# Kernel optimization log

Hardware: AMD Instinct MI355X
Metric: run time of the kernel (lower is better)

## Reference

```python
import jax, jax.numpy as jnp
import numpy as np

B, L, H, HD, FD = 1, 1024, 32, 64, 64
HID = H * HD
EPS = 1e-12


def setup_inputs() -> dict:
    key = jax.random.key(0)
    ks = jax.random.split(key, 7)
    s = 1.0 / np.sqrt(HID)
    return {
        "hidden_states": jax.random.normal(ks[0], (B, L, HID), dtype=jnp.float32),
        "Wq": jax.random.normal(ks[1], (HID, HID), dtype=jnp.float32) * s,
        "Wk": jax.random.normal(ks[2], (HID, HID), dtype=jnp.float32) * s,
        "Wv": jax.random.normal(ks[3], (HID, HID), dtype=jnp.float32) * s,
        "Wo": jax.random.normal(ks[4], (HID, HID), dtype=jnp.float32) * s,
        "Wfq": jax.random.normal(ks[5], (H, HD, FD), dtype=jnp.float32) * (1.0 / np.sqrt(HD)),
        "Wfk": jax.random.normal(ks[6], (H, HD, FD), dtype=jnp.float32) * (1.0 / np.sqrt(HD)),
    }


def _heads(x):
    # [b, l, hid] -> [b, h, l, hd]
    b, l, _ = x.shape
    return x.reshape(b, l, H, HD).transpose(0, 2, 1, 3)


def _feature_map(x, Wf):
    # per-head learned kernel + softmax over feature dim (hedgehog-style)
    z = jnp.einsum('bhld,hdf->bhlf', x, Wf)
    return jax.nn.softmax(z, axis=-1)


def _linear_attention(q, k, v, eps=EPS):
    # causal_dot_product: cumsum of outer-product KV state (fp32)
    qf, kf, vf = q.astype(jnp.float32), k.astype(jnp.float32), v.astype(jnp.float32)
    kv = jnp.cumsum(jnp.einsum('bhlf,bhld->bhlfd', kf, vf), axis=2)  # [b,h,l,f,d]
    y = jnp.einsum('bhlf,bhlfd->bhld', qf, kv)
    # fp32_attention=False branch: normalizer computed on cumsum(k)
    k_cum = jnp.cumsum(kf, axis=2).astype(q.dtype)
    denom = jnp.einsum('bhld,bhld->bhl', q, k_cum) + eps
    return y.astype(q.dtype) / denom[..., None]


def reference(hidden_states, Wq, Wk, Wv, Wo, Wfq, Wfk):
    b, l, _ = hidden_states.shape
    q = _heads(hidden_states @ Wq.T)
    k = _heads(hidden_states @ Wk.T)
    v = _heads(hidden_states @ Wv.T)
    fq = _feature_map(q, Wfq)
    fk = _feature_map(k, Wfk)
    y = _linear_attention(fq, fk, v)  # [b,h,l,hd]
    y = y.transpose(0, 2, 1, 3).reshape(b, l, HID)
    return y @ Wo.T
```

## Files before the change

### kernel.cpp

```cpp
#include <hip/hip_runtime.h>
#include <math.h>

constexpr int LQ  = 1024;
constexpr int NH  = 32;
constexpr int HDM = 64;
constexpr int FDM = 64;
constexpr int HID = 2048;
constexpr int NCH = 16;
constexpr int CT  = 64;
#define EPSV 1e-12f

typedef __bf16 bf16x8 __attribute__((ext_vector_type(8)));
typedef float  f32x4  __attribute__((ext_vector_type(4)));

__device__ __forceinline__ unsigned short f2b_raw(float x) {
    union { float f; unsigned int u; } v; v.f = x;
    unsigned int r = v.u + 0x7fffu + ((v.u >> 16) & 1u);
    return (unsigned short)(r >> 16);
}
__device__ __forceinline__ float b2f(ushort u) {
    union { unsigned int i; float f; } v; v.i = ((unsigned int)u) << 16; return v.f;
}

#define ASYNC16(ldsp, gp) __builtin_amdgcn_global_load_lds( \
    (const __attribute__((address_space(1))) void*)(gp),    \
    (__attribute__((address_space(3))) void*)(ldsp), 16, 0, 0)

template <int TM, int TN, bool BF16OUT>
__device__ __forceinline__ void gemm_core(const ushort* __restrict__ A,
                                          const ushort* __restrict__ B,
                                          void* __restrict__ Cv,
                                          int M, int N, int K) {
    constexpr int FI = TM / 32, FJ = TN / 32;
    constexpr int AI = TM / 32, BJ = TN / 32;
    constexpr int ASZ = TM * 64, BSZ = TN * 64;
    __shared__ __align__(16) ushort As[2 * ASZ];
    __shared__ __align__(16) ushort Bs[2 * BSZ];

    const int t = threadIdx.x, wave = t >> 6, lane = t & 63;
    const int wr = (wave >> 1) * (TM / 2), wc = (wave & 1) * (TN / 2);
    const int bm = blockIdx.y * TM, bn = blockIdx.x * TN;

    const int grow = lane >> 3;
    const int gsw  = ((lane & 7) ^ (grow & 7)) << 3;
    const int arow0 = wave * (TM / 4), brow0 = wave * (TN / 4);
    const ushort* gA = A + (size_t)(bm + arow0 + grow) * K + gsw;
    const ushort* gB = B + (size_t)(bn + brow0 + grow) * K + gsw;

    const int fr = lane & 15, q = lane >> 4;

    f32x4 acc[FI][FJ] = {};
    const int NIT = K >> 6;

    {
        ushort* ab = As + arow0 * 64;
        ushort* bb = Bs + brow0 * 64;
#pragma unroll
        for (int i = 0; i < AI; ++i) ASYNC16(ab + i * 512, gA + (size_t)i * 8 * K);
#pragma unroll
        for (int j = 0; j < BJ; ++j) ASYNC16(bb + j * 512, gB + (size_t)j * 8 * K);
    }
    __syncthreads();

    for (int it = 0; it < NIT; ++it) {
        const int p = it & 1;
        if (it + 1 < NIT) {
            const int ko = (it + 1) << 6;
            ushort* ab = As + (p ^ 1) * ASZ + arow0 * 64;
            ushort* bb = Bs + (p ^ 1) * BSZ + brow0 * 64;
#pragma unroll
            for (int i = 0; i < AI; ++i) ASYNC16(ab + i * 512, gA + ko + (size_t)i * 8 * K);
#pragma unroll
            for (int j = 0; j < BJ; ++j) ASYNC16(bb + j * 512, gB + ko + (size_t)j * 8 * K);
        }
        const ushort* ap = As + p * ASZ;
        const ushort* bp = Bs + p * BSZ;
        bf16x8 af[2][FI], bg[2][FJ];
#pragma unroll
        for (int ks = 0; ks < 2; ++ks) {
#pragma unroll
            for (int i = 0; i < FI; ++i) {
                const int row = wr + i * 16 + fr;
                af[ks][i] = *(const bf16x8*)&ap[row * 64 + ((((q + ks * 4)) ^ (row & 7)) << 3)];
            }
#pragma unroll
            for (int j = 0; j < FJ; ++j) {
                const int row = wc + j * 16 + fr;
                bg[ks][j] = *(const bf16x8*)&bp[row * 64 + ((((q + ks * 4)) ^ (row & 7)) << 3)];
            }
        }
#pragma unroll
        for (int ks = 0; ks < 2; ++ks)
#pragma unroll
            for (int i = 0; i < FI; ++i)
#pragma unroll
                for (int j = 0; j < FJ; ++j)
                    acc[i][j] = __builtin_amdgcn_mfma_f32_16x16x32_bf16(af[ks][i], bg[ks][j], acc[i][j], 0, 0, 0);
        if (it + 1 < NIT) __syncthreads();
    }

    const int er = q * 4;
    const int ec = lane & 15;
#pragma unroll
    for (int i = 0; i < FI; ++i)
#pragma unroll
        for (int j = 0; j < FJ; ++j) {
            const size_t base = (size_t)(bm + wr + i * 16 + er) * N + bn + wc + j * 16 + ec;
            if constexpr (BF16OUT) {
                ushort* C = (ushort*)Cv;
#pragma unroll
                for (int r = 0; r < 4; ++r) C[base + (size_t)r * N] = f2b_raw(acc[i][j][r]);
            } else {
                float* C = (float*)Cv;
#pragma unroll
                for (int r = 0; r < 4; ++r) C[base + (size_t)r * N] = acc[i][j][r];
            }
        }
}

__global__ __launch_bounds__(256) void gemm_qkv(const ushort* __restrict__ hsb,
                                                const ushort* __restrict__ wqb,
                                                const ushort* __restrict__ wkb,
                                                const ushort* __restrict__ wvb,
                                                ushort* __restrict__ qb,
                                                ushort* __restrict__ kb,
                                                ushort* __restrict__ vb) {
    const ushort* B; ushort* C;
    if (blockIdx.z == 0)      { B = wqb; C = qb; }
    else if (blockIdx.z == 1) { B = wkb; C = kb; }
    else                      { B = wvb; C = vb; }
    gemm_core<64, 128, true>(hsb, B, C, LQ, HID, HID);
}

__global__ __launch_bounds__(256) void gemm_one(const ushort* __restrict__ A,
                                                const ushort* __restrict__ B,
                                                float* __restrict__ C) {
    gemm_core<64, 64, false>(A, B, C, LQ, HID, HID);
}

struct F2BArgs { const float* src[5]; ushort* dst[5]; int n[5]; };
__global__ __launch_bounds__(256) void f2b_multi(F2BArgs p) {
    const int which = blockIdx.y;
    const float* s = p.src[which];
    ushort* d = p.dst[which];
    const int n = p.n[which];
    const int i = (blockIdx.x * 256 + threadIdx.x) * 4;
    if (i >= n) return;
    float4 v = *(const float4*)&s[i];
    ushort4 o = make_ushort4(f2b_raw(v.x), f2b_raw(v.y), f2b_raw(v.z), f2b_raw(v.w));
    *(ushort4*)&d[i] = o;
}

__global__ __launch_bounds__(256) void wf_transpose(const float* __restrict__ Wfq,
                                                    const float* __restrict__ Wfk,
                                                    ushort* __restrict__ WfqT,
                                                    ushort* __restrict__ WfkT) {
    const int h = blockIdx.x, isK = blockIdx.y;
    const float* src = (isK ? Wfk : Wfq) + (size_t)h * 4096;
    ushort* dst = (isK ? WfkT : WfqT) + (size_t)h * 4096;
    __shared__ float tile[64][65];
    const int t = threadIdx.x;
    for (int it = 0; it < 16; ++it) {
        int e = it * 256 + t; int d = e >> 6, f = e & 63;
        tile[d][f] = src[e];
    }
    __syncthreads();
    for (int it = 0; it < 16; ++it) {
        int e = it * 256 + t; int f = e >> 6, d = e & 63;
        dst[e] = f2b_raw(tile[d][f]);
    }
}

__global__ __launch_bounds__(256) void featmap_chunk(
    const ushort* __restrict__ qb, const ushort* __restrict__ kb,
    const ushort* __restrict__ vb,
    const ushort* __restrict__ WfqT, const ushort* __restrict__ WfkT,
    ushort* __restrict__ fqB, ushort* __restrict__ fkB,
    ushort* __restrict__ VTb, float* __restrict__ Sraw, float* __restrict__ Ks) {
    __shared__ __align__(16) ushort Xs[64 * 72];
    __shared__ __align__(16) ushort Ws[64 * 72];
    __shared__ float Zs[64][68];
    __shared__ __align__(16) ushort Fs[64 * 72];
    __shared__ __align__(16) ushort Vs[64 * 72];

    const int c = blockIdx.x, h = blockIdx.y, isK = blockIdx.z;
    const int t = threadIdx.x, lane = t & 63, wave = t >> 6;
    const int l0 = c * CT;
    const int fr = lane & 15, fo = (lane >> 4) * 8;
    const int g = lane >> 4, cc = lane & 15;

    const ushort* X  = (isK ? kb : qb);
    const ushort* WT = (isK ? WfkT : WfqT) + (size_t)h * 4096;

    for (int it = 0; it < 2; ++it) {
        int e = (it * 256 + t) * 8;
        int row = e >> 6, col = e & 63;
        *(uint4*)&Xs[row * 72 + col] = *(const uint4*)&X[(size_t)(l0 + row) * HID + h * HDM + col];
        *(uint4*)&Ws[row * 72 + col] = *(const uint4*)&WT[e];
        if (isK) {
            uint4 vv = *(const uint4*)&vb[(size_t)(l0 + row) * HID + h * HDM + col];
            const ushort* pv = (const ushort*)&vv;
#pragma unroll
            for (int i = 0; i < 8; ++i) Vs[(col + i) * 72 + row] = pv[i];
        }
    }
    __syncthreads();

    f32x4 accZ[4] = {};
#pragma unroll
    for (int kp = 0; kp < 2; ++kp) {
        bf16x8 a = *(const bf16x8*)&Xs[(wave * 16 + fr) * 72 + kp * 32 + fo];
#pragma unroll
        for (int j = 0; j < 4; ++j) {
            bf16x8 b = *(const bf16x8*)&Ws[(j * 16 + fr) * 72 + kp * 32 + fo];
            accZ[j] = __builtin_amdgcn_mfma_f32_16x16x32_bf16(a, b, accZ[j], 0, 0, 0);
        }
    }
#pragma unroll
    for (int j = 0; j < 4; ++j)
#pragma unroll
        for (int r = 0; r < 4; ++r)
            Zs[wave * 16 + g * 4 + r][j * 16 + cc] = accZ[j][r];
    __syncthreads();

    const int srow = t >> 2, spart = t & 3;
    float zv[16], m = -1e30f;
#pragma unroll
    for (int i = 0; i < 16; ++i) { zv[i] = Zs[srow][spart * 16 + i]; m = fmaxf(m, zv[i]); }
    m = fmaxf(m, __shfl_xor(m, 1)); m = fmaxf(m, __shfl_xor(m, 2));
    float s = 0.f;
#pragma unroll
    for (int i = 0; i < 16; ++i) { zv[i] = __expf(zv[i] - m); s += zv[i]; }
    s += __shfl_xor(s, 1); s += __shfl_xor(s, 2);
    const float inv = 1.0f / s;
    ushort ov[16];
#pragma unroll
    for (int i = 0; i < 16; ++i) ov[i] = f2b_raw(zv[i] * inv);
    ushort* outp = (isK ? fkB : fqB) + ((size_t)h * LQ + l0 + srow) * FDM + spart * 16;
    *(uint4*)&outp[0] = *(uint4*)&ov[0];
    *(uint4*)&outp[8] = *(uint4*)&ov[8];
    if (isK) {
#pragma unroll
        for (int i = 0; i < 16; ++i) Fs[(spart * 16 + i) * 72 + srow] = ov[i];
    }
    if (!isK) return;
    __syncthreads();

    if (t < 64) {
        float ks = 0.f;
#pragma unroll 8
        for (int l = 0; l < 64; ++l) ks += b2f(Fs[t * 72 + l]);
        Ks[((size_t)h * NCH + c) * FDM + t] = ks;
    }
    const size_t cb = ((size_t)h * NCH + c) * 4096;
    for (int it = 0; it < 2; ++it) {
        int e = (it * 256 + t) * 8;
        int row = e >> 6, col = e & 63;
        *(uint4*)&VTb[cb + e] = *(const uint4*)&Vs[row * 72 + col];
    }
    f32x4 accS[4] = {};
#pragma unroll
    for (int kp = 0; kp < 2; ++kp) {
        bf16x8 a = *(const bf16x8*)&Vs[(wave * 16 + fr) * 72 + kp * 32 + fo];
#pragma unroll
        for (int j = 0; j < 4; ++j) {
            bf16x8 b = *(const bf16x8*)&Fs[(j * 16 + fr) * 72 + kp * 32 + fo];
            accS[j] = __builtin_amdgcn_mfma_f32_16x16x32_bf16(a, b, accS[j], 0, 0, 0);
        }
    }
    float* sp = Sraw + cb;
#pragma unroll
    for (int j = 0; j < 4; ++j)
#pragma unroll
        for (int r = 0; r < 4; ++r)
            sp[(wave * 16 + g * 4 + r) * 64 + j * 16 + cc] = accS[j][r];
}

__global__ __launch_bounds__(256) void prefix2(const float* __restrict__ Sraw,
                                               ushort* __restrict__ SpreB,
                                               const float* __restrict__ Ks,
                                               float* __restrict__ Kpre) {
    const int h = blockIdx.x, eb = blockIdx.y, t = threadIdx.x;
    const int e0 = eb * 512 + t * 2;
    float r0 = 0.f, r1 = 0.f;
    const size_t hb = (size_t)h * NCH * 4096;
    for (int c2 = 0; c2 < NCH; ++c2) {
        const size_t base = hb + (size_t)c2 * 4096 + e0;
        float c0 = Sraw[base], c1 = Sraw[base + 1];
        ushort2 o = make_ushort2(f2b_raw(r0), f2b_raw(r1));
        *(ushort2*)&SpreB[base] = o;
        r0 += c0; r1 += c1;
    }
    if (eb == 0 && t < 64) {
        float rk = 0.f;
        for (int c2 = 0; c2 < NCH; ++c2) {
            const size_t kb2 = ((size_t)h * NCH + c2) * FDM + t;
            float cur = Ks[kb2];
            Kpre[kb2] = rk;
            rk += cur;
        }
    }
}

__global__ __launch_bounds__(256) void intra2(
    const ushort* __restrict__ fqB, const ushort* __restrict__ fkB,
    const ushort* __restrict__ VTb, const ushort* __restrict__ SpreB,
    const float* __restrict__ Kpre, ushort* __restrict__ Yb) {
    __shared__ __align__(16) ushort fqs[64 * 72];
    __shared__ __align__(16) ushort fks[64 * 72];
    __shared__ __align__(16) ushort VTs[64 * 72];
    __shared__ __align__(16) ushort Sps[64 * 72];
    __shared__ __align__(16) ushort Pms[64 * 72];
    __shared__ float den[64], kpr[64];

    const int c = blockIdx.x, h = blockIdx.y;
    const int t = threadIdx.x, lane = t & 63, wave = t >> 6;
    const int l0 = c * CT;
    const int fr = lane & 15, fo = (lane >> 4) * 8;
    const int g = lane >> 4, cc = lane & 15;

    const size_t qkbase = ((size_t)h * LQ + l0) * FDM;
    const size_t cbase  = ((size_t)h * NCH + c) * 4096;
    for (int it = 0; it < 2; ++it) {
        int e = (it * 256 + t) * 8;
        int row = e >> 6, col = e & 63;
        *(uint4*)&fqs[row * 72 + col] = *(const uint4*)&fqB[qkbase + e];
        *(uint4*)&fks[row * 72 + col] = *(const uint4*)&fkB[qkbase + e];
        *(uint4*)&VTs[row * 72 + col] = *(const uint4*)&VTb[cbase + e];
        *(uint4*)&Sps[row * 72 + col] = *(const uint4*)&SpreB[cbase + e];
    }
    if (t < 64) kpr[t] = Kpre[((size_t)h * NCH + c) * FDM + t];
    __syncthreads();

    f32x4 accP[4] = {};
#pragma unroll
    for (int kp = 0; kp < 2; ++kp) {
        bf16x8 a = *(const bf16x8*)&fqs[(wave * 16 + fr) * 72 + kp * 32 + fo];
#pragma unroll
        for (int j = 0; j < 4; ++j) {
            bf16x8 b = *(const bf16x8*)&fks[(j * 16 + fr) * 72 + kp * 32 + fo];
            accP[j] = __builtin_amdgcn_mfma_f32_16x16x32_bf16(a, b, accP[j], 0, 0, 0);
        }
    }
#pragma unroll
    for (int j = 0; j < 4; ++j)
#pragma unroll
        for (int r = 0; r < 4; ++r) {
            int l = wave * 16 + g * 4 + r, lp = j * 16 + cc;
            Pms[l * 72 + lp] = (lp <= l) ? f2b_raw(accP[j][r]) : (ushort)0;
        }
    __syncthreads();

    {
        const int srow = t >> 2, spart = t & 3;
        float s = 0.f;
#pragma unroll
        for (int i = 0; i < 16; ++i) s += b2f(Pms[srow * 72 + spart * 16 + i]);
#pragma unroll
        for (int i = 0; i < 16; ++i) s += b2f(fqs[srow * 72 + spart * 16 + i]) * kpr[spart * 16 + i];
        s += __shfl_xor(s, 1); s += __shfl_xor(s, 2);
        if (spart == 0) den[srow] = s + EPSV;
    }
    __syncthreads();

    f32x4 accY[4] = {};
#pragma unroll
    for (int kp = 0; kp < 2; ++kp) {
        bf16x8 a = *(const bf16x8*)&Pms[(wave * 16 + fr) * 72 + kp * 32 + fo];
#pragma unroll
        for (int j = 0; j < 4; ++j) {
            bf16x8 b = *(const bf16x8*)&VTs[(j * 16 + fr) * 72 + kp * 32 + fo];
            accY[j] = __builtin_amdgcn_mfma_f32_16x16x32_bf16(a, b, accY[j], 0, 0, 0);
        }
    }
#pragma unroll
    for (int kp = 0; kp < 2; ++kp) {
        bf16x8 a = *(const bf16x8*)&fqs[(wave * 16 + fr) * 72 + kp * 32 + fo];
#pragma unroll
        for (int j = 0; j < 4; ++j) {
            bf16x8 b = *(const bf16x8*)&Sps[(j * 16 + fr) * 72 + kp * 32 + fo];
            accY[j] = __builtin_amdgcn_mfma_f32_16x16x32_bf16(a, b, accY[j], 0, 0, 0);
        }
    }
#pragma unroll
    for (int r = 0; r < 4; ++r) {
        int l = wave * 16 + g * 4 + r;
        float inv = 1.0f / den[l];
        ushort* yo = Yb + (size_t)(l0 + l) * HID + h * HDM;
#pragma unroll
        for (int j = 0; j < 4; ++j)
            yo[j * 16 + cc] = f2b_raw(accY[j][r] * inv);
    }
}

extern "C" void kernel_launch(void* const* d_in, const int* in_sizes, int n_in,
                              void* d_out, int out_size, void* d_ws, size_t ws_size,
                              hipStream_t stream) {
    const float* hs  = (const float*)d_in[0];
    const float* Wq  = (const float*)d_in[1];
    const float* Wk  = (const float*)d_in[2];
    const float* Wv  = (const float*)d_in[3];
    const float* Wo  = (const float*)d_in[4];
    const float* Wfq = (const float*)d_in[5];
    const float* Wfk = (const float*)d_in[6];
    float* out = (float*)d_out;

    const size_t SZ = (size_t)LQ * HID;
    const size_t WZ = (size_t)HID * HID;

    char* w = (char*)d_ws;
    auto aus = [&](size_t n) { ushort* p = (ushort*)w; w += n * sizeof(ushort); return p; };
    auto afl = [&](size_t n) { float*  p = (float*)w;  w += n * sizeof(float);  return p; };

    ushort* hsb   = aus(SZ);
    ushort* wqb   = aus(WZ);
    ushort* wkb   = aus(WZ);
    ushort* wvb   = aus(WZ);
    ushort* wob   = aus(WZ);
    ushort* qb2   = aus(SZ);
    ushort* kb2   = aus(SZ);
    ushort* vb2   = aus(SZ);
    ushort* fqB   = aus(SZ);
    ushort* fkB   = aus(SZ);
    ushort* VTb   = aus(SZ);
    ushort* WfqT  = aus((size_t)NH * 4096);
    ushort* WfkT  = aus((size_t)NH * 4096);
    ushort* SpreB = aus(SZ);
    ushort* Yb    = aus(SZ);
    float*  Sraw  = afl(SZ);
    float*  Ks    = afl((size_t)NH * NCH * FDM);
    float*  Kpre  = afl((size_t)NH * NCH * FDM);

    F2BArgs fa;
    fa.src[0] = hs; fa.dst[0] = hsb; fa.n[0] = (int)SZ;
    fa.src[1] = Wq; fa.dst[1] = wqb; fa.n[1] = (int)WZ;
    fa.src[2] = Wk; fa.dst[2] = wkb; fa.n[2] = (int)WZ;
    fa.src[3] = Wv; fa.dst[3] = wvb; fa.n[3] = (int)WZ;
    fa.src[4] = Wo; fa.dst[4] = wob; fa.n[4] = (int)WZ;
    f2b_multi<<<dim3((unsigned)(WZ / 1024), 5), 256, 0, stream>>>(fa);

    wf_transpose<<<dim3(NH, 2), 256, 0, stream>>>(Wfq, Wfk, WfqT, WfkT);

    gemm_qkv<<<dim3(HID / 128, LQ / 64, 3), 256, 0, stream>>>(hsb, wqb, wkb, wvb, qb2, kb2, vb2);

    featmap_chunk<<<dim3(NCH, NH, 2), 256, 0, stream>>>(qb2, kb2, vb2, WfqT, WfkT,
                                                        fqB, fkB, VTb, Sraw, Ks);

    prefix2<<<dim3(NH, 8), 256, 0, stream>>>(Sraw, SpreB, Ks, Kpre);

    intra2<<<dim3(NCH, NH), 256, 0, stream>>>(fqB, fkB, VTb, SpreB, Kpre, Yb);

    gemm_one<<<dim3(HID / 64, LQ / 64), 256, 0, stream>>>(Yb, wob, out);
}
```

Measured before the change: 198.5 us.

## Fuse feature-map softmax into QKV GEMM epilogue and merge conversion kernels

```diff
diff --git a/kernel.cpp b/kernel.cpp
--- a/kernel.cpp
+++ b/kernel.cpp
@@ -81,12 +81,12 @@
 #pragma unroll
             for (int i = 0; i < FI; ++i) {
                 const int row = wr + i * 16 + fr;
-                af[ks][i] = *(const bf16x8*)&ap[row * 64 + ((((q + ks * 4)) ^ (row & 7)) << 3)];
+                af[ks][i] = *(const bf16x8*)&ap[row * 64 + (((q + ks * 4) ^ (row & 7)) << 3)];
             }
 #pragma unroll
             for (int j = 0; j < FJ; ++j) {
                 const int row = wc + j * 16 + fr;
-                bg[ks][j] = *(const bf16x8*)&bp[row * 64 + ((((q + ks * 4)) ^ (row & 7)) << 3)];
+                bg[ks][j] = *(const bf16x8*)&bp[row * 64 + (((q + ks * 4) ^ (row & 7)) << 3)];
             }
         }
 #pragma unroll
@@ -99,8 +99,7 @@
         if (it + 1 < NIT) __syncthreads();
     }
 
-    const int er = q * 4;
-    const int ec = lane & 15;
+    const int er = q * 4, ec = lane & 15;
 #pragma unroll
     for (int i = 0; i < FI; ++i)
 #pragma unroll
@@ -118,48 +117,189 @@
         }
 }
 
-__global__ __launch_bounds__(256) void gemm_qkv(const ushort* __restrict__ hsb,
-                                                const ushort* __restrict__ wqb,
-                                                const ushort* __restrict__ wkb,
-                                                const ushort* __restrict__ wvb,
-                                                ushort* __restrict__ qb,
-                                                ushort* __restrict__ kb,
-                                                ushort* __restrict__ vb) {
-    const ushort* B; ushort* C;
-    if (blockIdx.z == 0)      { B = wqb; C = qb; }
-    else if (blockIdx.z == 1) { B = wkb; C = kb; }
-    else                      { B = wvb; C = vb; }
-    gemm_core<64, 128, true>(hsb, B, C, LQ, HID, HID);
-}
-
 __global__ __launch_bounds__(256) void gemm_one(const ushort* __restrict__ A,
                                                 const ushort* __restrict__ B,
                                                 float* __restrict__ C) {
     gemm_core<64, 64, false>(A, B, C, LQ, HID, HID);
 }
 
-struct F2BArgs { const float* src[5]; ushort* dst[5]; int n[5]; };
-__global__ __launch_bounds__(256) void f2b_multi(F2BArgs p) {
-    const int which = blockIdx.y;
-    const float* s = p.src[which];
-    ushort* d = p.dst[which];
-    const int n = p.n[which];
-    const int i = (blockIdx.x * 256 + threadIdx.x) * 4;
-    if (i >= n) return;
-    float4 v = *(const float4*)&s[i];
-    ushort4 o = make_ushort4(f2b_raw(v.x), f2b_raw(v.y), f2b_raw(v.z), f2b_raw(v.w));
-    *(ushort4*)&d[i] = o;
-}
-
-__global__ __launch_bounds__(256) void wf_transpose(const float* __restrict__ Wfq,
-                                                    const float* __restrict__ Wfk,
-                                                    ushort* __restrict__ WfqT,
-                                                    ushort* __restrict__ WfkT) {
-    const int h = blockIdx.x, isK = blockIdx.y;
-    const float* src = (isK ? Wfk : Wfq) + (size_t)h * 4096;
-    ushort* dst = (isK ? WfkT : WfqT) + (size_t)h * 4096;
+__global__ __launch_bounds__(256) void gemm_qkv_fm(
+    const ushort* __restrict__ hsb,
+    const ushort* __restrict__ wqb, const ushort* __restrict__ wkb,
+    const ushort* __restrict__ wvb,
+    const ushort* __restrict__ WfqT, const ushort* __restrict__ WfkT,
+    ushort* __restrict__ fqB, ushort* __restrict__ fkB,
+    ushort* __restrict__ VTb) {
+    constexpr int TM = 64, TN = 128;
+    constexpr int ASZ = TM * 64, BSZ = TN * 64;
+    __shared__ __align__(16) ushort lds[2 * ASZ + 2 * BSZ];
+    ushort* As = lds;
+    ushort* Bs = lds + 2 * ASZ;
+
+    const int z = blockIdx.z;
+    const ushort* Bmat = (z == 0) ? wqb : (z == 1) ? wkb : wvb;
+
+    const int t = threadIdx.x, wave = t >> 6, lane = t & 63;
+    const int wr = (wave >> 1) * 32, wc = (wave & 1) * 64;
+    const int bx = blockIdx.x, c = blockIdx.y;
+    const int bm = c * TM, bn = bx * TN, l0 = c * CT;
+
+    const int grow = lane >> 3;
+    const int gsw  = ((lane & 7) ^ (grow & 7)) << 3;
+    const int arow0 = wave * 16, brow0 = wave * 32;
+    const ushort* gA = hsb  + (size_t)(bm + arow0 + grow) * HID + gsw;
+    const ushort* gB = Bmat + (size_t)(bn + brow0 + grow) * HID + gsw;
+
+    const int fr = lane & 15, q = lane >> 4, ec = lane & 15;
+
+    f32x4 acc[2][4] = {};
+    const int NIT = HID >> 6;
+
+    {
+        ushort* ab = As + arow0 * 64;
+        ushort* bb = Bs + brow0 * 64;
+#pragma unroll
+        for (int i = 0; i < 2; ++i) ASYNC16(ab + i * 512, gA + (size_t)i * 8 * HID);
+#pragma unroll
+        for (int j = 0; j < 4; ++j) ASYNC16(bb + j * 512, gB + (size_t)j * 8 * HID);
+    }
+    __syncthreads();
+
+    for (int it = 0; it < NIT; ++it) {
+        const int p = it & 1;
+        if (it + 1 < NIT) {
+            const int ko = (it + 1) << 6;
+            ushort* ab = As + (p ^ 1) * ASZ + arow0 * 64;
+            ushort* bb = Bs + (p ^ 1) * BSZ + brow0 * 64;
+#pragma unroll
+            for (int i = 0; i < 2; ++i) ASYNC16(ab + i * 512, gA + ko + (size_t)i * 8 * HID);
+#pragma unroll
+            for (int j = 0; j < 4; ++j) ASYNC16(bb + j * 512, gB + ko + (size_t)j * 8 * HID);
+        }
+        const ushort* ap = As + p * ASZ;
+        const ushort* bp = Bs + p * BSZ;
+        bf16x8 af[2][2], bg[2][4];
+#pragma unroll
+        for (int ks = 0; ks < 2; ++ks) {
+#pragma unroll
+            for (int i = 0; i < 2; ++i) {
+                const int row = wr + i * 16 + fr;
+                af[ks][i] = *(const bf16x8*)&ap[row * 64 + (((q + ks * 4) ^ (row & 7)) << 3)];
+            }
+#pragma unroll
+            for (int j = 0; j < 4; ++j) {
+                const int row = wc + j * 16 + fr;
+                bg[ks][j] = *(const bf16x8*)&bp[row * 64 + (((q + ks * 4) ^ (row & 7)) << 3)];
+            }
+        }
+#pragma unroll
+        for (int ks = 0; ks < 2; ++ks)
+#pragma unroll
+            for (int i = 0; i < 2; ++i)
+#pragma unroll
+                for (int j = 0; j < 4; ++j)
+                    acc[i][j] = __builtin_amdgcn_mfma_f32_16x16x32_bf16(af[ks][i], bg[ks][j], acc[i][j], 0, 0, 0);
+        if (it + 1 < NIT) __syncthreads();
+    }
+
+    if (z == 2) {
+#pragma unroll
+        for (int i = 0; i < 2; ++i)
+#pragma unroll
+            for (int j = 0; j < 4; ++j) {
+                const int col = wc + j * 16 + ec;
+                const int hh = col >> 6, d = col & 63;
+                const int lb = wr + i * 16 + q * 4;
+                const size_t base = (((size_t)(2 * bx + hh) * NCH + c) * 64 + d) * 64 + lb;
+                ushort4 o = make_ushort4(f2b_raw(acc[i][j][0]), f2b_raw(acc[i][j][1]),
+                                         f2b_raw(acc[i][j][2]), f2b_raw(acc[i][j][3]));
+                *(ushort4*)&VTb[base] = o;
+            }
+        return;
+    }
+
+    __syncthreads();
+    ushort* Qt  = lds;
+    ushort* Wfs = lds + 8704;
+#pragma unroll
+    for (int i = 0; i < 2; ++i)
+#pragma unroll
+        for (int j = 0; j < 4; ++j)
+#pragma unroll
+            for (int r = 0; r < 4; ++r)
+                Qt[(wr + i * 16 + q * 4 + r) * 136 + wc + j * 16 + ec] = f2b_raw(acc[i][j][r]);
+    {
+        const ushort* WT = ((z == 0) ? WfqT : WfkT) + (size_t)(2 * bx) * 4096;
+#pragma unroll
+        for (int it = 0; it < 4; ++it) {
+            const int e = it * 2048 + t * 8;
+            const int hh = e >> 12, f = (e >> 6) & 63, dc = e & 63;
+            uint4 wv4 = *(const uint4*)&WT[e];
+            *(uint4*)&Wfs[hh * 4608 + f * 72 + dc] = wv4;
+        }
+    }
+    __syncthreads();
+
+    const int hh = wave & 1, R0 = (wave >> 1) * 32;
+    f32x4 z2[2][4] = {};
+#pragma unroll
+    for (int ks = 0; ks < 2; ++ks) {
+        bf16x8 a[2];
+#pragma unroll
+        for (int i = 0; i < 2; ++i)
+            a[i] = *(const bf16x8*)&Qt[(R0 + i * 16 + fr) * 136 + hh * 64 + ks * 32 + q * 8];
+#pragma unroll
+        for (int j = 0; j < 4; ++j) {
+            bf16x8 b = *(const bf16x8*)&Wfs[hh * 4608 + (j * 16 + fr) * 72 + ks * 32 + q * 8];
+#pragma unroll
+            for (int i = 0; i < 2; ++i)
+                z2[i][j] = __builtin_amdgcn_mfma_f32_16x16x32_bf16(a[i], b, z2[i][j], 0, 0, 0);
+        }
+    }
+
+    ushort* outp = (z == 0) ? fqB : fkB;
+    const int hgl = 2 * bx + hh;
+#pragma unroll
+    for (int i = 0; i < 2; ++i)
+#pragma unroll
+        for (int r = 0; r < 4; ++r) {
+            float m = z2[i][0][r];
+#pragma unroll
+            for (int j = 1; j < 4; ++j) m = fmaxf(m, z2[i][j][r]);
+            m = fmaxf(m, __shfl_xor(m, 1)); m = fmaxf(m, __shfl_xor(m, 2));
+            m = fmaxf(m, __shfl_xor(m, 4)); m = fmaxf(m, __shfl_xor(m, 8));
+            float e4[4], s = 0.f;
+#pragma unroll
+            for (int j = 0; j < 4; ++j) { e4[j] = __expf(z2[i][j][r] - m); s += e4[j]; }
+            s += __shfl_xor(s, 1); s += __shfl_xor(s, 2);
+            s += __shfl_xor(s, 4); s += __shfl_xor(s, 8);
+            const float inv = 1.0f / s;
+            const int l = R0 + i * 16 + q * 4 + r;
+            ushort* op = outp + ((size_t)hgl * LQ + l0 + l) * FDM;
+#pragma unroll
+            for (int j = 0; j < 4; ++j) op[j * 16 + ec] = f2b_raw(e4[j] * inv);
+        }
+}
+
+struct ConvArgs {
+    const float* src[5]; ushort* dst[5]; int n[5];
+    const float* Wfq; const float* Wfk; ushort* WfqT; ushort* WfkT;
+};
+__global__ __launch_bounds__(256) void conv_all(ConvArgs p) {
+    const int y = blockIdx.y, t = threadIdx.x;
+    if (y < 5) {
+        const int i = (blockIdx.x * 256 + t) * 4;
+        if (i >= p.n[y]) return;
+        float4 v = *(const float4*)&p.src[y][i];
+        ushort4 o = make_ushort4(f2b_raw(v.x), f2b_raw(v.y), f2b_raw(v.z), f2b_raw(v.w));
+        *(ushort4*)&p.dst[y][i] = o;
+        return;
+    }
+    if (blockIdx.x >= NH) return;
+    const int h = blockIdx.x;
+    const float* src = ((y == 6) ? p.Wfk : p.Wfq) + (size_t)h * 4096;
+    ushort* dst = ((y == 6) ? p.WfkT : p.WfqT) + (size_t)h * 4096;
     __shared__ float tile[64][65];
-    const int t = threadIdx.x;
     for (int it = 0; it < 16; ++it) {
         int e = it * 256 + t; int d = e >> 6, f = e & 63;
         tile[d][f] = src[e];
@@ -171,109 +311,50 @@
     }
 }
 
-__global__ __launch_bounds__(256) void featmap_chunk(
-    const ushort* __restrict__ qb, const ushort* __restrict__ kb,
-    const ushort* __restrict__ vb,
-    const ushort* __restrict__ WfqT, const ushort* __restrict__ WfkT,
-    ushort* __restrict__ fqB, ushort* __restrict__ fkB,
-    ushort* __restrict__ VTb, float* __restrict__ Sraw, float* __restrict__ Ks) {
-    __shared__ __align__(16) ushort Xs[64 * 72];
-    __shared__ __align__(16) ushort Ws[64 * 72];
-    __shared__ float Zs[64][68];
+__global__ __launch_bounds__(256) void chunk_state(
+    const ushort* __restrict__ fkB, const ushort* __restrict__ VTb,
+    float* __restrict__ Sraw, float* __restrict__ Ks) {
+    __shared__ __align__(16) ushort Vs[64 * 72];
     __shared__ __align__(16) ushort Fs[64 * 72];
-    __shared__ __align__(16) ushort Vs[64 * 72];
-
-    const int c = blockIdx.x, h = blockIdx.y, isK = blockIdx.z;
-    const int t = threadIdx.x, lane = t & 63, wave = t >> 6;
+    const int c = blockIdx.x, h = blockIdx.y;
+    const int t = threadIdx.x, lane = t & 63, w = t >> 6;
     const int l0 = c * CT;
-    const int fr = lane & 15, fo = (lane >> 4) * 8;
-    const int g = lane >> 4, cc = lane & 15;
-
-    const ushort* X  = (isK ? kb : qb);
-    const ushort* WT = (isK ? WfkT : WfqT) + (size_t)h * 4096;
+    const int fr = lane & 15, q = lane >> 4, ec = lane & 15;
+    const size_t cb = ((size_t)h * NCH + c) * 4096;
 
     for (int it = 0; it < 2; ++it) {
-        int e = (it * 256 + t) * 8;
-        int row = e >> 6, col = e & 63;
-        *(uint4*)&Xs[row * 72 + col] = *(const uint4*)&X[(size_t)(l0 + row) * HID + h * HDM + col];
-        *(uint4*)&Ws[row * 72 + col] = *(const uint4*)&WT[e];
-        if (isK) {
-            uint4 vv = *(const uint4*)&vb[(size_t)(l0 + row) * HID + h * HDM + col];
-            const ushort* pv = (const ushort*)&vv;
-#pragma unroll
-            for (int i = 0; i < 8; ++i) Vs[(col + i) * 72 + row] = pv[i];
-        }
-    }
-    __syncthreads();
-
-    f32x4 accZ[4] = {};
-#pragma unroll
-    for (int kp = 0; kp < 2; ++kp) {
-        bf16x8 a = *(const bf16x8*)&Xs[(wave * 16 + fr) * 72 + kp * 32 + fo];
+        const int e = (it * 256 + t) * 8;
+        const int row = e >> 6, col = e & 63;
+        *(uint4*)&Vs[row * 72 + col] = *(const uint4*)&VTb[cb + e];
+        uint4 fv = *(const uint4*)&fkB[((size_t)h * LQ + l0) * FDM + e];
+        const ushort* pf = (const ushort*)&fv;
+#pragma unroll
+        for (int i2 = 0; i2 < 8; ++i2) Fs[(col + i2) * 72 + row] = pf[i2];
+    }
+    __syncthreads();
+
+    f32x4 acc[4] = {};
+#pragma unroll
+    for (int ks = 0; ks < 2; ++ks) {
+        bf16x8 a = *(const bf16x8*)&Vs[(w * 16 + fr) * 72 + ks * 32 + q * 8];
 #pragma unroll
         for (int j = 0; j < 4; ++j) {
-            bf16x8 b = *(const bf16x8*)&Ws[(j * 16 + fr) * 72 + kp * 32 + fo];
-            accZ[j] = __builtin_amdgcn_mfma_f32_16x16x32_bf16(a, b, accZ[j], 0, 0, 0);
-        }
-    }
+            bf16x8 b = *(const bf16x8*)&Fs[(j * 16 + fr) * 72 + ks * 32 + q * 8];
+            acc[j] = __builtin_amdgcn_mfma_f32_16x16x32_bf16(a, b, acc[j], 0, 0, 0);
+        }
+    }
+    float* sp = Sraw + cb;
 #pragma unroll
     for (int j = 0; j < 4; ++j)
 #pragma unroll
         for (int r = 0; r < 4; ++r)
-            Zs[wave * 16 + g * 4 + r][j * 16 + cc] = accZ[j][r];
-    __syncthreads();
-
-    const int srow = t >> 2, spart = t & 3;
-    float zv[16], m = -1e30f;
-#pragma unroll
-    for (int i = 0; i < 16; ++i) { zv[i] = Zs[srow][spart * 16 + i]; m = fmaxf(m, zv[i]); }
-    m = fmaxf(m, __shfl_xor(m, 1)); m = fmaxf(m, __shfl_xor(m, 2));
-    float s = 0.f;
-#pragma unroll
-    for (int i = 0; i < 16; ++i) { zv[i] = __expf(zv[i] - m); s += zv[i]; }
-    s += __shfl_xor(s, 1); s += __shfl_xor(s, 2);
-    const float inv = 1.0f / s;
-    ushort ov[16];
-#pragma unroll
-    for (int i = 0; i < 16; ++i) ov[i] = f2b_raw(zv[i] * inv);
-    ushort* outp = (isK ? fkB : fqB) + ((size_t)h * LQ + l0 + srow) * FDM + spart * 16;
-    *(uint4*)&outp[0] = *(uint4*)&ov[0];
-    *(uint4*)&outp[8] = *(uint4*)&ov[8];
-    if (isK) {
-#pragma unroll
-        for (int i = 0; i < 16; ++i) Fs[(spart * 16 + i) * 72 + srow] = ov[i];
-    }
-    if (!isK) return;
-    __syncthreads();
-
+            sp[(w * 16 + q * 4 + r) * 64 + j * 16 + ec] = acc[j][r];
     if (t < 64) {
-        float ks = 0.f;
+        float s = 0.f;
 #pragma unroll 8
-        for (int l = 0; l < 64; ++l) ks += b2f(Fs[t * 72 + l]);
-        Ks[((size_t)h * NCH + c) * FDM + t] = ks;
-    }
-    const size_t cb = ((size_t)h * NCH + c) * 4096;
-    for (int it = 0; it < 2; ++it) {
-        int e = (it * 256 + t) * 8;
-        int row = e >> 6, col = e & 63;
-        *(uint4*)&VTb[cb + e] = *(const uint4*)&Vs[row * 72 + col];
-    }
-    f32x4 accS[4] = {};
-#pragma unroll
-    for (int kp = 0; kp < 2; ++kp) {
-        bf16x8 a = *(const bf16x8*)&Vs[(wave * 16 + fr) * 72 + kp * 32 + fo];
-#pragma unroll
-        for (int j = 0; j < 4; ++j) {
-            bf16x8 b = *(const bf16x8*)&Fs[(j * 16 + fr) * 72 + kp * 32 + fo];
-            accS[j] = __builtin_amdgcn_mfma_f32_16x16x32_bf16(a, b, accS[j], 0, 0, 0);
-        }
-    }
-    float* sp = Sraw + cb;
-#pragma unroll
-    for (int j = 0; j < 4; ++j)
-#pragma unroll
-        for (int r = 0; r < 4; ++r)
-            sp[(wave * 16 + g * 4 + r) * 64 + j * 16 + cc] = accS[j][r];
+        for (int l = 0; l < 64; ++l) s += b2f(Fs[t * 72 + l]);
+        Ks[((size_t)h * NCH + c) * FDM + t] = s;
+    }
 }
 
 __global__ __launch_bounds__(256) void prefix2(const float* __restrict__ Sraw,
@@ -417,9 +498,6 @@
     ushort* wkb   = aus(WZ);
     ushort* wvb   = aus(WZ);
     ushort* wob   = aus(WZ);
-    ushort* qb2   = aus(SZ);
-    ushort* kb2   = aus(SZ);
-    ushort* vb2   = aus(SZ);
     ushort* fqB   = aus(SZ);
     ushort* fkB   = aus(SZ);
     ushort* VTb   = aus(SZ);
@@ -431,20 +509,19 @@
     float*  Ks    = afl((size_t)NH * NCH * FDM);
     float*  Kpre  = afl((size_t)NH * NCH * FDM);
 
-    F2BArgs fa;
-    fa.src[0] = hs; fa.dst[0] = hsb; fa.n[0] = (int)SZ;
-    fa.src[1] = Wq; fa.dst[1] = wqb; fa.n[1] = (int)WZ;
-    fa.src[2] = Wk; fa.dst[2] = wkb; fa.n[2] = (int)WZ;
-    fa.src[3] = Wv; fa.dst[3] = wvb; fa.n[3] = (int)WZ;
-    fa.src[4] = Wo; fa.dst[4] = wob; fa.n[4] = (int)WZ;
-    f2b_multi<<<dim3((unsigned)(WZ / 1024), 5), 256, 0, stream>>>(fa);
-
-    wf_transpose<<<dim3(NH, 2), 256, 0, stream>>>(Wfq, Wfk, WfqT, WfkT);
-
-    gemm_qkv<<<dim3(HID / 128, LQ / 64, 3), 256, 0, stream>>>(hsb, wqb, wkb, wvb, qb2, kb2, vb2);
-
-    featmap_chunk<<<dim3(NCH, NH, 2), 256, 0, stream>>>(qb2, kb2, vb2, WfqT, WfkT,
-                                                        fqB, fkB, VTb, Sraw, Ks);
+    ConvArgs ca;
+    ca.src[0] = hs; ca.dst[0] = hsb; ca.n[0] = (int)SZ;
+    ca.src[1] = Wq; ca.dst[1] = wqb; ca.n[1] = (int)WZ;
+    ca.src[2] = Wk; ca.dst[2] = wkb; ca.n[2] = (int)WZ;
+    ca.src[3] = Wv; ca.dst[3] = wvb; ca.n[3] = (int)WZ;
+    ca.src[4] = Wo; ca.dst[4] = wob; ca.n[4] = (int)WZ;
+    ca.Wfq = Wfq; ca.Wfk = Wfk; ca.WfqT = WfqT; ca.WfkT = WfkT;
+    conv_all<<<dim3((unsigned)(WZ / 1024), 7), 256, 0, stream>>>(ca);
+
+    gemm_qkv_fm<<<dim3(HID / 128, LQ / 64, 3), 256, 0, stream>>>(
+        hsb, wqb, wkb, wvb, WfqT, WfkT, fqB, fkB, VTb);
+
+    chunk_state<<<dim3(NCH, NH), 256, 0, stream>>>(fkB, VTb, Sraw, Ks);
 
     prefix2<<<dim3(NH, 8), 256, 0, stream>>>(Sraw, SpreB, Ks, Kpre);
 
```

New measurement: 195.2 us (median of 2 runs). No clear change (-1.6%).
